# Performance work log

Measured on AMD Instinct MI355X. Metric: run time of the kernel, lower is better.

Reference implementation:

```python
import jax, jax.numpy as jnp
import numpy as np

B, T, E, H, D, NL = 2, 1024, 2048, 16, 128, 3
MAXL = T * (2 ** (NL - 1))  # k length doubles each layer: T, 2T, 4T


def _rms_norm(x, w, eps=1e-5):
    return x * jax.lax.rsqrt(jnp.mean(x * x, axis=-1, keepdims=True) + eps) * w


def _rope(x, cos, sin):
    # x: [B, S, H, D]; cos/sin: [>=S, D/2]; GPT-NeoX style (non-interleaved)
    S = x.shape[1]
    c = cos[:S][None, :, None, :]
    s = sin[:S][None, :, None, :]
    x1, x2 = jnp.split(x, 2, axis=-1)
    return jnp.concatenate([x1 * c - x2 * s, x1 * s + x2 * c], axis=-1)


def _causal_attn(q, k, v):
    # bottom-right-aligned causal (flash_attn_func causal=True with kv longer than q)
    Tq, L = q.shape[1], k.shape[1]
    scale = 1.0 / np.sqrt(q.shape[-1]).astype(np.float32)
    scores = jnp.einsum('bthd,bshd->bhts', q, k) * scale
    i = jnp.arange(Tq)[:, None]
    j = jnp.arange(L)[None, :]
    mask = j <= i + (L - Tq)
    scores = jnp.where(mask[None, None], scores, -jnp.inf)
    p = jax.nn.softmax(scores, axis=-1)
    return jnp.einsum('bhts,bshd->bthd', p, v)


def setup_inputs() -> dict:
    key = jax.random.key(0)
    ks = jax.random.split(key, 6)
    x = jax.random.normal(ks[0], (B, T, E), dtype=jnp.float32)
    inv_freq = 1.0 / (10000.0 ** (np.arange(0, D, 2, dtype=np.float32) / D))  # [D/2]
    ang = np.arange(MAXL, dtype=np.float32)[:, None] * inv_freq[None, :]      # [MAXL, D/2]
    cos = jnp.asarray(np.cos(ang), dtype=jnp.float32)
    sin = jnp.asarray(np.sin(ang), dtype=jnp.float32)
    wq = jax.random.normal(ks[1], (NL, E, E), dtype=jnp.float32) * 0.02
    wk = jax.random.normal(ks[2], (NL, E, E), dtype=jnp.float32) * 0.02
    wv = jax.random.normal(ks[3], (NL, E, E), dtype=jnp.float32) * 0.02
    ln_w = jnp.ones((NL, E), dtype=jnp.float32)
    lambdas = jnp.zeros((NL,), dtype=jnp.float32)
    w_out = jax.random.normal(ks[4], (E, E), dtype=jnp.float32) * 0.02
    final_ln_w = jnp.ones((E,), dtype=jnp.float32)
    alpha = jnp.ones((1,), dtype=jnp.float32)
    return {'x': x, 'cos': cos, 'sin': sin, 'wq': wq, 'wk': wk, 'wv': wv,
            'ln_w': ln_w, 'lambdas': lambdas, 'w_out': w_out,
            'final_ln_w': final_ln_w, 'alpha': alpha}


def reference(x, cos, sin, wq, wk, wv, ln_w, lambdas, w_out, final_ln_w, alpha):
    bsz, tgt_len, embed_dim = x.shape
    # lambda weights: sigmoid then LayerNorm over the NL scalars (no affine)
    lam = jax.nn.sigmoid(lambdas)
    lam = (lam - jnp.mean(lam)) * jax.lax.rsqrt(jnp.var(lam) + 1e-5)
    acc_k, acc_v = [], []
    total = jnp.zeros_like(x)
    for i in range(NL):  # small fixed layer count
        q = (x @ wq[i].T).reshape(bsz, tgt_len, H, D)
        k = (x @ wk[i].T).reshape(bsz, tgt_len, H, D)
        v = (x @ wv[i].T).reshape(bsz, tgt_len, H, D)
        if i > 0:
            k = jnp.concatenate([k] + acc_k, axis=1)
            v = jnp.concatenate([v] + acc_v, axis=1)
        q = _rope(q, cos, sin)
        k = _rope(k, cos, sin)  # note: cached K gets rotary re-applied, as in source
        attn = _causal_attn(q, k, v).reshape(bsz, tgt_len, embed_dim)
        attn = _rms_norm(attn, ln_w[i])
        total = total + attn * lam[i]
        acc_k.append(k)
        acc_v.append(v)
    out = _rms_norm(total + alpha * x, final_ln_w)
    return out @ w_out.T
```

## Files before the change

### kernel.cpp

```cpp
#include <hip/hip_runtime.h>
#include <hip/hip_bf16.h>

typedef unsigned short ushort_t;
typedef __attribute__((ext_vector_type(8))) short bf16x8;
typedef __attribute__((ext_vector_type(4))) short bf16x4;
typedef __attribute__((ext_vector_type(4))) float f32x4;
typedef __attribute__((ext_vector_type(4))) unsigned short u16x4;
typedef __attribute__((ext_vector_type(4))) unsigned int u32x4;

#define DEV __device__ __forceinline__

DEV ushort_t f2bf(float f) {
  __hip_bfloat16 h = __float2bfloat16(f);
  return __builtin_bit_cast(unsigned short, h);
}
DEV float bf2f(ushort_t b) {
  union { float f; unsigned int u; } a; a.u = ((unsigned int)b) << 16;
  return a.f;
}
DEV void gload_lds16(const void* g, void* l) {
  __builtin_amdgcn_global_load_lds((const __attribute__((address_space(1))) void*)g,
                                   (__attribute__((address_space(3))) void*)l, 16, 0, 0);
}
DEV unsigned ldsaddr(const void* l) {
  return (unsigned)(unsigned long long)(const __attribute__((address_space(3))) void*)l;
}
template <int OFF>
DEV bf16x4 tr16o(unsigned a) {
  bf16x4 d;
  asm volatile("ds_read_b64_tr_b16 %0, %1 offset:%c2" : "=v"(d) : "v"(a), "i"(OFF));
  return d;
}
template <int OFF>
DEV bf16x8 ldsb128o(unsigned a) {
  bf16x8 d;
  asm volatile("ds_read_b128 %0, %1 offset:%c2" : "=v"(d) : "v"(a), "i"(OFF));
  return d;
}

__global__ __launch_bounds__(256) void f2b_kernel(const float* __restrict__ in,
                                                  ushort_t* __restrict__ out, int n) {
  int base = (blockIdx.x * 256 + threadIdx.x) * 4;
  if (base >= n) return;
  f32x4 v = *(const f32x4*)(in + base);
  u16x4 o;
  o.x = f2bf(v.x); o.y = f2bf(v.y); o.z = f2bf(v.z); o.w = f2bf(v.w);
  *(u16x4*)(out + base) = o;
}

__global__ __launch_bounds__(256) void f2b3_kernel(const float* __restrict__ a, const float* __restrict__ b,
                                                   const float* __restrict__ c, ushort_t* __restrict__ out) {
  int id = blockIdx.x * 256 + threadIdx.x;
  int sel = id >> 20, k = (id & 1048575) * 4;
  const float* src = sel == 0 ? a : sel == 1 ? b : c;
  f32x4 v = *(const f32x4*)(src + k);
  u16x4 o;
  o.x = f2bf(v.x); o.y = f2bf(v.y); o.z = f2bf(v.z); o.w = f2bf(v.w);
  *(u16x4*)(out + (size_t)sel * 4194304 + k) = o;
}

__global__ void lam_kernel(const float* __restrict__ lambdas, float* __restrict__ lam) {
  if (threadIdx.x == 0 && blockIdx.x == 0) {
    float l0 = 1.f / (1.f + __expf(-lambdas[0]));
    float l1 = 1.f / (1.f + __expf(-lambdas[1]));
    float l2 = 1.f / (1.f + __expf(-lambdas[2]));
    float mean = (l0 + l1 + l2) * (1.f / 3.f);
    float d0 = l0 - mean, d1 = l1 - mean, d2 = l2 - mean;
    float var = (d0 * d0 + d1 * d1 + d2 * d2) * (1.f / 3.f);
    float rs = rsqrtf(var + 1e-5f);
    lam[0] = d0 * rs; lam[1] = d1 * rs; lam[2] = d2 * rs;
  }
}

DEV void gemm_core(const ushort_t* __restrict__ A, const ushort_t* __restrict__ Bm,
                   ushort_t* lsA, ushort_t* lsB, int bm, int bn, int kbeg, int kend,
                   f32x4 (&acc)[4][4]) {
  const int K = 2048;
  int tid = threadIdx.x;
  int w = tid >> 6, lane = tid & 63;
  int g = lane >> 4, r = lane & 15;
  int wm = w >> 1, wn = w & 1;
#pragma unroll
  for (int i = 0; i < 4; ++i)
#pragma unroll
    for (int j = 0; j < 4; ++j) acc[i][j] = 0.f;

  for (int kk = kbeg; kk < kend; kk += 32) {
    __syncthreads();
#pragma unroll
    for (int j2 = 0; j2 < 2; ++j2) {
      int eb = w * 1024 + j2 * 512;
      int ebl = eb + lane * 8;
      int rr = ebl >> 5, cc = ebl & 31;
      gload_lds16(A + (size_t)(bm * 128 + rr) * K + kk + cc, lsA + eb);
      gload_lds16(Bm + (size_t)(bn * 128 + rr) * K + kk + cc, lsB + eb);
    }
    __syncthreads();
    bf16x8 af[4], bfr[4];
#pragma unroll
    for (int i = 0; i < 4; ++i)
      af[i] = *(const bf16x8*)(lsA + (wm * 64 + i * 16 + r) * 32 + g * 8);
#pragma unroll
    for (int j = 0; j < 4; ++j)
      bfr[j] = *(const bf16x8*)(lsB + (wn * 64 + j * 16 + r) * 32 + g * 8);
#pragma unroll
    for (int i = 0; i < 4; ++i)
#pragma unroll
      for (int j = 0; j < 4; ++j)
        acc[i][j] = __builtin_amdgcn_mfma_f32_16x16x32_bf16(af[i], bfr[j], acc[i][j], 0, 0, 0);
  }
}

#define MM(i, j)                                                                              \
  acc[i][j] = __builtin_amdgcn_mfma_f32_16x16x32_bf16(af[(i) & 3][0], bfr[j][0], acc[i][j], 0, 0, 0); \
  acc[i][j] = __builtin_amdgcn_mfma_f32_16x16x32_bf16(af[(i) & 3][1], bfr[j][1], acc[i][j], 0, 0, 0);

__global__ __launch_bounds__(512, 2) void gemm_qkv256(
    const ushort_t* __restrict__ A,
    const ushort_t* __restrict__ Bq, const ushort_t* __restrict__ Bk, const ushort_t* __restrict__ Bv,
    ushort_t* __restrict__ Cq, ushort_t* __restrict__ Ck, ushort_t* __restrict__ Cv, int Lkv) {
  __shared__ __align__(16) ushort_t lsA[32768];
  __shared__ __align__(16) ushort_t lsB[32768];
  const int NT = 32;

  int bid = (int)blockIdx.x;
  int swz = (bid & 7) * 24 + (bid >> 3);
  int bm = swz / 24;
  int rest = swz % 24;
  int sel = rest >> 3, bnc = rest & 7;
  const ushort_t* Bmat = (sel == 0) ? Bq : (sel == 1) ? Bk : Bv;
  ushort_t* C = (sel == 0) ? Cq : (sel == 1) ? Ck : Cv;
  int Lsel = (sel == 0) ? 1024 : Lkv;

  int tid = threadIdx.x;
  int wv = tid >> 6, lane = tid & 63;
  int wm = wv >> 2, wn = wv & 3;
  int g = lane >> 4, r = lane & 15;

  int row0 = tid >> 3, c0 = tid & 7;
  int colsw = (c0 ^ (row0 & 7)) * 8;
  const ushort_t* pA0 = A + (size_t)(bm * 256 + row0) * 2048 + colsw;
  const ushort_t* pB0 = Bmat + (size_t)(bnc * 256 + row0) * 2048 + colsw;
  ushort_t* dA = lsA + tid * 8;
  ushort_t* dB = lsB + tid * 8;

  auto SA = [&](int T, int hh) {
    const ushort_t* s = pA0 + (size_t)(hh * 128) * 2048 + (size_t)T * 64;
    ushort_t* d = dA + (T & 1) * 16384 + hh * 8192;
    gload_lds16(s, d);
    gload_lds16(s + (size_t)64 * 2048, d + 4096);
  };
  auto SB = [&](int T, int hh) {
    const ushort_t* s = pB0 + (size_t)(hh * 128) * 2048 + (size_t)T * 64;
    ushort_t* d = dB + (T & 1) * 16384 + hh * 8192;
    gload_lds16(s, d);
    gload_lds16(s + (size_t)64 * 2048, d + 4096);
  };

  unsigned xm = (unsigned)(r & 7);
  unsigned aAb = ldsaddr(lsA) + (unsigned)((wm * 128 + r) * 128);
  unsigned aA0b = aAb + ((((unsigned)g) ^ xm) << 4);
  unsigned aA1b = aAb + ((((unsigned)(4 + g)) ^ xm) << 4);
  unsigned aBb = ldsaddr(lsB) + (unsigned)((wn * 64 + r) * 128);
  unsigned aB0b = aBb + ((((unsigned)g) ^ xm) << 4);
  unsigned aB1b = aBb + ((((unsigned)(4 + g)) ^ xm) << 4);

  f32x4 acc[8][4];
#pragma unroll
  for (int i = 0; i < 8; ++i)
#pragma unroll
    for (int j = 0; j < 4; ++j) acc[i][j] = 0.f;
  bf16x8 af[4][2], bfr[4][2];

  SA(0, 0); SB(0, 0); SB(0, 1); SA(0, 1);
  SA(1, 0); SB(1, 0); SB(1, 1);
  asm volatile("s_waitcnt vmcnt(6)" ::: "memory");
  __builtin_amdgcn_s_barrier();
  __builtin_amdgcn_sched_barrier(0);

  for (int t = 0; t < NT; ++t) {
    unsigned cb = (unsigned)((t & 1) << 15);
    unsigned A0 = aA0b + cb, A1 = aA1b + cb, B0 = aB0b + cb, B1 = aB1b + cb;
    bool full = (t < NT - 2);
    af[0][0] = ldsb128o<0>(A0);     af[0][1] = ldsb128o<0>(A1);
    af[1][0] = ldsb128o<2048>(A0);  af[1][1] = ldsb128o<2048>(A1);
    af[2][0] = ldsb128o<4096>(A0);  af[2][1] = ldsb128o<4096>(A1);
    af[3][0] = ldsb128o<6144>(A0);  af[3][1] = ldsb128o<6144>(A1);
    bfr[0][0] = ldsb128o<0>(B0);    bfr[0][1] = ldsb128o<0>(B1);
    bfr[1][0] = ldsb128o<2048>(B0); bfr[1][1] = ldsb128o<2048>(B1);
    if (t + 1 < NT) SA(t + 1, 1);
    __builtin_amdgcn_s_barrier();
    asm volatile("s_waitcnt lgkmcnt(0)" ::: "memory");
    __builtin_amdgcn_sched_barrier(0);
    __builtin_amdgcn_s_setprio(1);
    MM(0, 0) MM(1, 0) MM(2, 0) MM(3, 0) MM(0, 1) MM(1, 1) MM(2, 1) MM(3, 1)
    __builtin_amdgcn_s_setprio(0);
    __builtin_amdgcn_sched_barrier(0);
    __builtin_amdgcn_s_barrier();
    bfr[2][0] = ldsb128o<4096>(B0); bfr[2][1] = ldsb128o<4096>(B1);
    bfr[3][0] = ldsb128o<6144>(B0); bfr[3][1] = ldsb128o<6144>(B1);
    if (full) SA(t + 2, 0);
    __builtin_amdgcn_s_barrier();
    asm volatile("s_waitcnt lgkmcnt(0)" ::: "memory");
    __builtin_amdgcn_sched_barrier(0);
    __builtin_amdgcn_s_setprio(1);
    MM(0, 2) MM(1, 2) MM(2, 2) MM(3, 2) MM(0, 3) MM(1, 3) MM(2, 3) MM(3, 3)
    __builtin_amdgcn_s_setprio(0);
    if (full) { asm volatile("s_waitcnt vmcnt(4)" ::: "memory"); }
    else      { asm volatile("s_waitcnt vmcnt(0)" ::: "memory"); }
    __builtin_amdgcn_sched_barrier(0);
    __builtin_amdgcn_s_barrier();
    af[0][0] = ldsb128o<8192>(A0);  af[0][1] = ldsb128o<8192>(A1);
    af[1][0] = ldsb128o<10240>(A0); af[1][1] = ldsb128o<10240>(A1);
    af[2][0] = ldsb128o<12288>(A0); af[2][1] = ldsb128o<12288>(A1);
    af[3][0] = ldsb128o<14336>(A0); af[3][1] = ldsb128o<14336>(A1);
    if (full) SB(t + 2, 0);
    __builtin_amdgcn_s_barrier();
    asm volatile("s_waitcnt lgkmcnt(0)" ::: "memory");
    __builtin_amdgcn_sched_barrier(0);
    __builtin_amdgcn_s_setprio(1);
    MM(4, 2) MM(5, 2) MM(6, 2) MM(7, 2) MM(4, 3) MM(5, 3) MM(6, 3) MM(7, 3)
    __builtin_amdgcn_s_setprio(0);
    __builtin_amdgcn_sched_barrier(0);
    __builtin_amdgcn_s_barrier();
    if (full) SB(t + 2, 1);
    __builtin_amdgcn_s_barrier();
    __builtin_amdgcn_s_setprio(1);
    MM(4, 0) MM(5, 0) MM(6, 0) MM(7, 0) MM(4, 1) MM(5, 1) MM(6, 1) MM(7, 1)
    __builtin_amdgcn_s_setprio(0);
    if (full) { asm volatile("s_waitcnt vmcnt(8)" ::: "memory"); }
    else      { asm volatile("s_waitcnt vmcnt(0)" ::: "memory"); }
    __builtin_amdgcn_sched_barrier(0);
    __builtin_amdgcn_s_barrier();
  }

  int prow = bm * 256 + wm * 128 + g * 4;
  int pcol = bnc * 256 + wn * 64 + r;
#pragma unroll
  for (int i = 0; i < 8; ++i)
#pragma unroll
    for (int j = 0; j < 4; ++j) {
      int col = pcol + j * 16;
#pragma unroll
      for (int tt = 0; tt < 4; ++tt) {
        int row = prow + i * 16 + tt;
        int b2 = row >> 10, t2 = row & 1023;
        C[(size_t)(b2 * Lsel + t2) * 2048 + col] = f2bf(acc[i][j][tt]);
      }
    }
}
#undef MM

__global__ __launch_bounds__(256) void gemm_bt_part(
    const ushort_t* __restrict__ A, const ushort_t* __restrict__ Bm, float* __restrict__ P) {
  __shared__ __align__(16) ushort_t lsA[4096];
  __shared__ __align__(16) ushort_t lsB[4096];
  int bn = blockIdx.x, bm = blockIdx.y, s = blockIdx.z;
  f32x4 acc[4][4];
  gemm_core(A, Bm, lsA, lsB, bm, bn, s * 1024, (s + 1) * 1024, acc);
  float* C = P + (size_t)s * 4194304;
  int lane = threadIdx.x & 63, w = threadIdx.x >> 6;
  int g = lane >> 4, r = lane & 15, wm = w >> 1, wn = w & 1;
#pragma unroll
  for (int i = 0; i < 4; ++i)
#pragma unroll
    for (int j = 0; j < 4; ++j) {
      int row0 = bm * 128 + wm * 64 + i * 16 + g * 4;
      int col = bn * 128 + wn * 64 + j * 16 + r;
#pragma unroll
      for (int t = 0; t < 4; ++t)
        C[(size_t)(row0 + t) * 2048 + col] = acc[i][j][t];
    }
}

__global__ __launch_bounds__(256) void add2_kernel(const float* __restrict__ a, const float* __restrict__ b,
                                                   float* __restrict__ out) {
  int i = (blockIdx.x * 256 + threadIdx.x) * 4;
  f32x4 va = *(const f32x4*)(a + i);
  f32x4 vb = *(const f32x4*)(b + i);
  f32x4 r;
#pragma unroll
  for (int k = 0; k < 4; ++k) r[k] = va[k] + vb[k];
  *(f32x4*)(out + i) = r;
}

DEV void rope_body(const ushort_t* src, ushort_t* dst, const float* cosT, const float* sinT,
                   int Ls, int s0, int Ld, int dpos0, int cnt, int bp) {
  int b = bp / cnt, pidx = bp % cnt;
  int pos = dpos0 + pidx;
  int pi = threadIdx.x * 4;
  int h = pi >> 6, d = pi & 63;
  const ushort_t* s_ = src + ((size_t)(b * Ls + s0 + pidx) * 16 + h) * 128 + d;
  ushort_t* d_ = dst + ((size_t)(b * Ld + pos) * 16 + h) * 128 + d;
  f32x4 c4 = *(const f32x4*)(cosT + (size_t)pos * 64 + d);
  f32x4 s4 = *(const f32x4*)(sinT + (size_t)pos * 64 + d);
  u16x4 x1 = *(const u16x4*)(s_);
  u16x4 x2 = *(const u16x4*)(s_ + 64);
  u16x4 o1, o2;
#pragma unroll
  for (int k = 0; k < 4; ++k) {
    float a = bf2f(x1[k]), bb = bf2f(x2[k]);
    o1[k] = f2bf(a * c4[k] - bb * s4[k]);
    o2[k] = f2bf(a * s4[k] + bb * c4[k]);
  }
  *(u16x4*)d_ = o1;
  *(u16x4*)(d_ + 64) = o2;
}
DEV void copy_body(const ushort_t* src, ushort_t* dst, int Ls, int s0, int Ld, int dpos0,
                   int cnt, int bp) {
  int b = bp / cnt, pidx = bp % cnt;
  const u32x4* s = (const u32x4*)(src + (size_t)(b * Ls + s0 + pidx) * 2048);
  u32x4* d = (u32x4*)(dst + (size_t)(b * Ld + dpos0 + pidx) * 2048);
  d[threadIdx.x] = s[threadIdx.x];
}

__global__ __launch_bounds__(256) void rope_k(ushort_t* Kc, const float* __restrict__ cosT,
                                              const float* __restrict__ sinT, int L) {
  rope_body(Kc, Kc, cosT, sinT, L, 0, L, 0, 1024, blockIdx.x);
}

__global__ __launch_bounds__(256) void layer1_cache(const ushort_t* __restrict__ K0, ushort_t* __restrict__ K1,
                                                    const ushort_t* __restrict__ V0, ushort_t* __restrict__ V1,
                                                    const float* __restrict__ cosT, const float* __restrict__ sinT) {
  int bp = blockIdx.x;
  if (bp < 2048) rope_body(K0, K1, cosT, sinT, 1024, 0, 2048, 1024, 1024, bp);
  else copy_body(V0, V1, 1024, 0, 2048, 1024, 1024, bp - 2048);
}

__global__ __launch_bounds__(256) void layer2_cache(const ushort_t* __restrict__ K1, ushort_t* __restrict__ K2,
                                                    const ushort_t* __restrict__ V1, ushort_t* __restrict__ V2,
                                                    const float* __restrict__ cosT, const float* __restrict__ sinT) {
  int bp = blockIdx.x;
  if (bp < 2048) copy_body(K1, K2, 2048, 1024, 4096, 1024, 1024, bp);
  else if (bp < 6144) rope_body(K1, K2, cosT, sinT, 2048, 0, 4096, 2048, 2048, bp - 2048);
  else if (bp < 8192) copy_body(V1, V2, 2048, 1024, 4096, 1024, 1024, bp - 6144);
  else copy_body(V1, V2, 2048, 0, 4096, 2048, 2048, bp - 8192);
}

__global__ __launch_bounds__(256, 4) void attn_kernel(
    const ushort_t* __restrict__ Qraw, const ushort_t* __restrict__ Kc, const ushort_t* __restrict__ Vc,
    const float* __restrict__ cosT, const float* __restrict__ sinT,
    ushort_t* __restrict__ Opart, float2* __restrict__ Ml, int Lk) {
  __shared__ __align__(16) ushort_t lsK[8192];
  __shared__ __align__(16) ushort_t lsV[8192];
  const float SC2 = 0.1275174366f;

  int bid = (int)blockIdx.x;
  int swz = (bid & 7) * 128 + (bid >> 3);
  int s = swz & 1;
  int rest = swz >> 1;

  int w = threadIdx.x >> 6, lane = threadIdx.x & 63;
  int bq = rest & 15, h = (rest >> 4) & 15, b = rest >> 8;
  int qt = bq * 4 + w;
  int g = lane >> 4, r = lane & 15;
  int off = Lk - 1024;

  const ushort_t* qbase = Qraw + ((size_t)(b * 1024 + qt * 16 + r) * 16 + h) * 128;
  int pos = qt * 16 + r;
  const float* cb = cosT + (size_t)pos * 64;
  const float* sb = sinT + (size_t)pos * 64;
  bf16x8 qf[4];
#pragma unroll
  for (int c = 0; c < 2; ++c) {
    int d0 = c * 32 + g * 8;
    f32x4 c0 = *(const f32x4*)(cb + d0);
    f32x4 c1 = *(const f32x4*)(cb + d0 + 4);
    f32x4 s0 = *(const f32x4*)(sb + d0);
    f32x4 s1 = *(const f32x4*)(sb + d0 + 4);
    bf16x8 x1 = *(const bf16x8*)(qbase + d0);
    bf16x8 x2 = *(const bf16x8*)(qbase + d0 + 64);
    bf16x8 lo, hi;
#pragma unroll
    for (int k = 0; k < 8; ++k) {
      float cv = (k < 4 ? c0[k] : c1[k - 4]) * SC2;
      float sv = (k < 4 ? s0[k] : s1[k - 4]) * SC2;
      float a = bf2f((ushort_t)x1[k]);
      float bb = bf2f((ushort_t)x2[k]);
      lo[k] = (short)f2bf(a * cv - bb * sv);
      hi[k] = (short)f2bf(a * sv + bb * cv);
    }
    qf[c] = lo; qf[c + 2] = hi;
  }

  int t = threadIdx.x;
  int krow0 = t >> 4,        kc0 = (t & 15) ^ (krow0 & 7);
  int krow1 = (t + 256) >> 4, kc1 = (t & 15) ^ (krow1 & 7);
  const size_t adv = 32 * 2048;
  const size_t adv2 = 2 * adv;
  const ushort_t* srcK0 = Kc + ((size_t)(b * Lk + krow0) * 16 + h) * 128 + kc0 * 8 + s * adv;
  const ushort_t* srcK1 = Kc + ((size_t)(b * Lk + krow1) * 16 + h) * 128 + kc1 * 8 + s * adv;
  int L0 = t, L1 = t + 256;
  int vrow0 = ((L0 >> 3) & 7) * 4 + ((L0 >> 1) & 3), vd0 = (L0 >> 6) * 16 + (L0 & 1) * 8;
  int vrow1 = ((L1 >> 3) & 7) * 4 + ((L1 >> 1) & 3), vd1 = (L1 >> 6) * 16 + (L1 & 1) * 8;
  const ushort_t* srcV0 = Vc + ((size_t)(b * Lk + vrow0) * 16 + h) * 128 + vd0 + s * adv;
  const ushort_t* srcV1 = Vc + ((size_t)(b * Lk + vrow1) * 16 + h) * 128 + vd1 + s * adv;

  auto STAGE = [&](int buf) {
    ushort_t* k0 = lsK + buf * 4096 + w * 512;
    ushort_t* v0 = lsV + buf * 4096 + w * 512;
    gload_lds16(srcK0, k0);
    gload_lds16(srcK1, k0 + 2048);
    gload_lds16(srcV0, v0);
    gload_lds16(srcV1, v0 + 2048);
    srcK0 += adv2; srcK1 += adv2; srcV0 += adv2; srcV1 += adv2;
  };

  unsigned kx[4];
  unsigned kbase0 = ldsaddr(lsK) + (unsigned)(r * 256);
#pragma unroll
  for (int c = 0; c < 4; ++c)
    kx[c] = kbase0 + (unsigned)((((c * 32 + g * 8) ^ ((r & 7) * 8))) * 2);
  unsigned vbase0 = ldsaddr(lsV);

  float m_run = -1e30f, l_run = 0.f;
  f32x4 o[8];
#pragma unroll
  for (int c = 0; c < 8; ++c) o[c] = 0.f;

  int qp = qt * 16 + r + off;
  int qmin = qt * 16 + off;
  int nkt_w = ((qt * 16 + 15 + off) >> 5) + 1;
  int nkt_blk = (((bq * 4 + 3) * 16 + 15 + off) >> 5) + 1;
  int ntile = (nkt_blk - s + 1) >> 1;

#define LDK(c, ks) ldsb128o<(ks) * 4096>(kx[c] + kb)
#define LDV(hh, i) tr16o<(hh) * 4096 + (i) * 512>(vb)

  if (ntile > 0) {
    STAGE(0);
    for (int it = 0; it < ntile; ++it) {
      int kt = s + it * 2;
      int cur = it & 1;
      if (it + 1 < ntile) {
        STAGE(cur ^ 1);
        asm volatile("s_waitcnt vmcnt(4)" ::: "memory");
      } else {
        asm volatile("s_waitcnt vmcnt(0)" ::: "memory");
      }
      __builtin_amdgcn_s_barrier();
      __builtin_amdgcn_sched_barrier(0);
      if (kt < nkt_w) {
        unsigned kb = (unsigned)(cur << 13);
        unsigned vb = vbase0 + kb;
        f32x4 st[2];
        {
          bf16x8 k0 = LDK(0, 0), k1 = LDK(1, 0), k2 = LDK(2, 0), k3 = LDK(3, 0);
          asm volatile("s_waitcnt lgkmcnt(0)" ::: "memory");
          __builtin_amdgcn_sched_barrier(0);
          __builtin_amdgcn_s_setprio(1);
          f32x4 acc = 0.f;
          acc = __builtin_amdgcn_mfma_f32_16x16x32_bf16(k0, qf[0], acc, 0, 0, 0);
          acc = __builtin_amdgcn_mfma_f32_16x16x32_bf16(k1, qf[1], acc, 0, 0, 0);
          acc = __builtin_amdgcn_mfma_f32_16x16x32_bf16(k2, qf[2], acc, 0, 0, 0);
          acc = __builtin_amdgcn_mfma_f32_16x16x32_bf16(k3, qf[3], acc, 0, 0, 0);
          __builtin_amdgcn_s_setprio(0);
          st[0] = acc;
        }
        {
          bf16x8 k0 = LDK(0, 1), k1 = LDK(1, 1), k2 = LDK(2, 1), k3 = LDK(3, 1);
          asm volatile("s_waitcnt lgkmcnt(0)" ::: "memory");
          __builtin_amdgcn_sched_barrier(0);
          __builtin_amdgcn_s_setprio(1);
          f32x4 acc = 0.f;
          acc = __builtin_amdgcn_mfma_f32_16x16x32_bf16(k0, qf[0], acc, 0, 0, 0);
          acc = __builtin_amdgcn_mfma_f32_16x16x32_bf16(k1, qf[1], acc, 0, 0, 0);
          acc = __builtin_amdgcn_mfma_f32_16x16x32_bf16(k2, qf[2], acc, 0, 0, 0);
          acc = __builtin_amdgcn_mfma_f32_16x16x32_bf16(k3, qf[3], acc, 0, 0, 0);
          __builtin_amdgcn_s_setprio(0);
          st[1] = acc;
        }
        float pmax = -1e30f;
        int kp0 = kt * 32;
        if (kp0 + 31 > qmin) {
#pragma unroll
          for (int ks = 0; ks < 2; ++ks)
#pragma unroll
            for (int j = 0; j < 4; ++j) {
              int key = kp0 + ks * 16 + g * 4 + j;
              float sv = st[ks][j];
              if (key > qp) sv = -1e30f;
              st[ks][j] = sv;
              pmax = fmaxf(pmax, sv);
            }
        } else {
#pragma unroll
          for (int ks = 0; ks < 2; ++ks)
#pragma unroll
            for (int j = 0; j < 4; ++j) pmax = fmaxf(pmax, st[ks][j]);
        }
        pmax = fmaxf(pmax, __shfl_xor(pmax, 16, 64));
        pmax = fmaxf(pmax, __shfl_xor(pmax, 32, 64));
        if (!__all(pmax <= m_run + 11.5f)) {
          float mnew = fmaxf(m_run, pmax);
          float corr = exp2f(m_run - mnew);
          l_run *= corr;
#pragma unroll
          for (int c = 0; c < 8; ++c)
#pragma unroll
            for (int tt = 0; tt < 4; ++tt) o[c][tt] *= corr;
          m_run = mnew;
        }
        float psum = 0.f;
        bf16x4 pf[2];
#pragma unroll
        for (int ks = 0; ks < 2; ++ks)
#pragma unroll
          for (int j = 0; j < 4; ++j) {
            float pe = exp2f(st[ks][j] - m_run);
            psum += pe;
            pf[ks][j] = (short)f2bf(pe);
          }
        psum += __shfl_xor(psum, 16, 64);
        psum += __shfl_xor(psum, 32, 64);
        l_run += psum;
        {
          bf16x4 v0 = LDV(0, 0), v1 = LDV(0, 1), v2 = LDV(0, 2), v3 = LDV(0, 3);
          bf16x4 v4 = LDV(0, 4), v5 = LDV(0, 5), v6 = LDV(0, 6), v7 = LDV(0, 7);
          asm volatile("s_waitcnt lgkmcnt(0)" ::: "memory");
          __builtin_amdgcn_sched_barrier(0);
          __builtin_amdgcn_s_setprio(1);
          o[0] = __builtin_amdgcn_mfma_f32_16x16x16bf16_1k(v0, pf[0], o[0], 0, 0, 0);
          o[0] = __builtin_amdgcn_mfma_f32_16x16x16bf16_1k(v1, pf[1], o[0], 0, 0, 0);
          o[1] = __builtin_amdgcn_mfma_f32_16x16x16bf16_1k(v2, pf[0], o[1], 0, 0, 0);
          o[1] = __builtin_amdgcn_mfma_f32_16x16x16bf16_1k(v3, pf[1], o[1], 0, 0, 0);
          o[2] = __builtin_amdgcn_mfma_f32_16x16x16bf16_1k(v4, pf[0], o[2], 0, 0, 0);
          o[2] = __builtin_amdgcn_mfma_f32_16x16x16bf16_1k(v5, pf[1], o[2], 0, 0, 0);
          o[3] = __builtin_amdgcn_mfma_f32_16x16x16bf16_1k(v6, pf[0], o[3], 0, 0, 0);
          o[3] = __builtin_amdgcn_mfma_f32_16x16x16bf16_1k(v7, pf[1], o[3], 0, 0, 0);
          __builtin_amdgcn_s_setprio(0);
        }
        {
          bf16x4 v0 = LDV(1, 0), v1 = LDV(1, 1), v2 = LDV(1, 2), v3 = LDV(1, 3);
          bf16x4 v4 = LDV(1, 4), v5 = LDV(1, 5), v6 = LDV(1, 6), v7 = LDV(1, 7);
          asm volatile("s_waitcnt lgkmcnt(0)" ::: "memory");
          __builtin_amdgcn_sched_barrier(0);
          __builtin_amdgcn_s_setprio(1);
          o[4] = __builtin_amdgcn_mfma_f32_16x16x16bf16_1k(v0, pf[0], o[4], 0, 0, 0);
          o[4] = __builtin_amdgcn_mfma_f32_16x16x16bf16_1k(v1, pf[1], o[4], 0, 0, 0);
          o[5] = __builtin_amdgcn_mfma_f32_16x16x16bf16_1k(v2, pf[0], o[5], 0, 0, 0);
          o[5] = __builtin_amdgcn_mfma_f32_16x16x16bf16_1k(v3, pf[1], o[5], 0, 0, 0);
          o[6] = __builtin_amdgcn_mfma_f32_16x16x16bf16_1k(v4, pf[0], o[6], 0, 0, 0);
          o[6] = __builtin_amdgcn_mfma_f32_16x16x16bf16_1k(v5, pf[1], o[6], 0, 0, 0);
          o[7] = __builtin_amdgcn_mfma_f32_16x16x16bf16_1k(v6, pf[0], o[7], 0, 0, 0);
          o[7] = __builtin_amdgcn_mfma_f32_16x16x16bf16_1k(v7, pf[1], o[7], 0, 0, 0);
          __builtin_amdgcn_s_setprio(0);
        }
      }
      __builtin_amdgcn_sched_barrier(0);
      __builtin_amdgcn_s_barrier();
    }
  }
#undef LDK
#undef LDV
  ushort_t* ob = Opart + (size_t)s * 4194304 + ((size_t)(b * 1024 + qt * 16 + r) * 16 + h) * 128;
#pragma unroll
  for (int dblk = 0; dblk < 8; ++dblk) {
    u16x4 ov;
#pragma unroll
    for (int tt = 0; tt < 4; ++tt) ov[tt] = f2bf(o[dblk][tt]);
    *(u16x4*)(ob + dblk * 16 + g * 4) = ov;
  }
  if (g == 0) {
    float2 ml; ml.x = m_run; ml.y = l_run;
    Ml[((size_t)(s * 2 + b) * 1024 + qt * 16 + r) * 16 + h] = ml;
  }
}

template <int FIRST>
__global__ __launch_bounds__(256) void rms_combine(const ushort_t* __restrict__ Opart, const float2* __restrict__ Ml,
                                                   const float* __restrict__ lnw, const float* __restrict__ lam,
                                                   int li, float* __restrict__ total) {
  int row = blockIdx.x;
  int t8 = threadIdx.x * 8;
  int h = t8 >> 7;
  float2 ml0 = Ml[(size_t)row * 16 + h];
  float2 ml1 = Ml[(size_t)(row + 2048) * 16 + h];
  float M = fmaxf(ml0.x, ml1.x);
  float w0 = exp2f(ml0.x - M), w1 = exp2f(ml1.x - M);
  float rinv = 1.f / (w0 * ml0.y + w1 * ml1.y);
  w0 *= rinv; w1 *= rinv;
  const ushort_t* a0 = Opart + (size_t)row * 2048 + t8;
  const ushort_t* a1 = a0 + 4194304;
  u16x4 p00 = *(const u16x4*)(a0);
  u16x4 p01 = *(const u16x4*)(a0 + 4);
  u16x4 p10 = *(const u16x4*)(a1);
  u16x4 p11 = *(const u16x4*)(a1 + 4);
  f32x4 v0, v1;
#pragma unroll
  for (int k = 0; k < 4; ++k) {
    v0[k] = w0 * bf2f(p00[k]) + w1 * bf2f(p10[k]);
    v1[k] = w0 * bf2f(p01[k]) + w1 * bf2f(p11[k]);
  }
  float ss = v0.x * v0.x + v0.y * v0.y + v0.z * v0.z + v0.w * v0.w +
             v1.x * v1.x + v1.y * v1.y + v1.z * v1.z + v1.w * v1.w;
#pragma unroll
  for (int m = 1; m < 64; m <<= 1) ss += __shfl_xor(ss, m, 64);
  __shared__ float red[4];
  int w = threadIdx.x >> 6, lane = threadIdx.x & 63;
  if (lane == 0) red[w] = ss;
  __syncthreads();
  ss = red[0] + red[1] + red[2] + red[3];
  float sca = rsqrtf(ss * (1.f / 2048.f) + 1e-5f) * lam[li];
  f32x4 w0v = *(const f32x4*)(lnw + t8);
  f32x4 w1v = *(const f32x4*)(lnw + t8 + 4);
  float* o = total + (size_t)row * 2048 + t8;
  f32x4 r0, r1;
#pragma unroll
  for (int k = 0; k < 4; ++k) { r0[k] = v0[k] * sca * w0v[k]; r1[k] = v1[k] * sca * w1v[k]; }
  if (!FIRST) {
    f32x4 q0 = *(const f32x4*)(o);
    f32x4 q1 = *(const f32x4*)(o + 4);
#pragma unroll
    for (int k = 0; k < 4; ++k) { r0[k] += q0[k]; r1[k] += q1[k]; }
  }
  *(f32x4*)(o) = r0;
  *(f32x4*)(o + 4) = r1;
}

__global__ __launch_bounds__(256) void final_norm(const float* __restrict__ total, const float* __restrict__ x,
                                                  const float* __restrict__ alphap, const float* __restrict__ flw,
                                                  ushort_t* __restrict__ ybf) {
  int row = blockIdx.x;
  float al = alphap[0];
  int t8 = threadIdx.x * 8;
  const float* tp = total + (size_t)row * 2048 + t8;
  const float* xp = x + (size_t)row * 2048 + t8;
  f32x4 t0 = *(const f32x4*)(tp);
  f32x4 t1 = *(const f32x4*)(tp + 4);
  f32x4 x0 = *(const f32x4*)(xp);
  f32x4 x1 = *(const f32x4*)(xp + 4);
  float y[8];
#pragma unroll
  for (int k = 0; k < 4; ++k) { y[k] = t0[k] + al * x0[k]; y[4 + k] = t1[k] + al * x1[k]; }
  float ss = 0.f;
#pragma unroll
  for (int k = 0; k < 8; ++k) ss += y[k] * y[k];
#pragma unroll
  for (int m = 1; m < 64; m <<= 1) ss += __shfl_xor(ss, m, 64);
  __shared__ float red[4];
  int w = threadIdx.x >> 6, lane = threadIdx.x & 63;
  if (lane == 0) red[w] = ss;
  __syncthreads();
  ss = red[0] + red[1] + red[2] + red[3];
  float s = rsqrtf(ss * (1.f / 2048.f) + 1e-5f);
  f32x4 w0 = *(const f32x4*)(flw + t8);
  f32x4 w1 = *(const f32x4*)(flw + t8 + 4);
  u16x4 o0, o1;
#pragma unroll
  for (int k = 0; k < 4; ++k) {
    o0[k] = f2bf(y[k] * s * w0[k]);
    o1[k] = f2bf(y[4 + k] * s * w1[k]);
  }
  *(u16x4*)(ybf + (size_t)row * 2048 + t8) = o0;
  *(u16x4*)(ybf + (size_t)row * 2048 + t8 + 4) = o1;
}

extern "C" void kernel_launch(void* const* d_in, const int* in_sizes, int n_in,
                              void* d_out, int out_size, void* d_ws, size_t ws_size,
                              hipStream_t stream) {
  const float* x = (const float*)d_in[0];
  const float* cosT = (const float*)d_in[1];
  const float* sinT = (const float*)d_in[2];
  const float* wq = (const float*)d_in[3];
  const float* wk = (const float*)d_in[4];
  const float* wv = (const float*)d_in[5];
  const float* lnw = (const float*)d_in[6];
  const float* lambdas = (const float*)d_in[7];
  const float* w_out = (const float*)d_in[8];
  const float* flw = (const float*)d_in[9];
  const float* alpha = (const float*)d_in[10];

  const size_t ME = 4194304ull;
  char* p = (char*)d_ws;
  size_t off = 0;
  auto alc = [&](size_t bytes) -> void* {
    void* r = p + off;
    off += (bytes + 255) & ~(size_t)255;
    return r;
  };
  ushort_t* xb = (ushort_t*)alc(ME * 2);
  void* uni = alc(2 * ME * 4);
  ushort_t* wl = (ushort_t*)uni;
  ushort_t* Opart = (ushort_t*)uni;
  float* Ppart = (float*)uni;
  ushort_t* q = (ushort_t*)alc(ME * 2);
  ushort_t* K0 = (ushort_t*)alc(ME * 2);
  ushort_t* K1 = (ushort_t*)alc(2 * ME * 2);
  ushort_t* K2 = (ushort_t*)alc(4 * ME * 2);
  ushort_t* V0 = (ushort_t*)alc(ME * 2);
  ushort_t* V1 = (ushort_t*)alc(2 * ME * 2);
  ushort_t* V2 = (ushort_t*)alc(4 * ME * 2);
  float* total = (float*)alc(ME * 4);
  float2* Ml = (float2*)alc(65536 * 8);
  float* lam = (float*)alc(256);
  ushort_t* ybf = q;
  ushort_t* wob = K0;

  f2b_kernel<<<4096, 256, 0, stream>>>(x, xb, 4194304);
  lam_kernel<<<1, 64, 0, stream>>>(lambdas, lam);

  ushort_t* Kc[3] = {K0, K1, K2};
  ushort_t* Vc[3] = {V0, V1, V2};

  for (int li = 0; li < 3; ++li) {
    int L = 1024 << li;
    size_t woff = (size_t)li * ME;
    f2b3_kernel<<<12288, 256, 0, stream>>>(wq + woff, wk + woff, wv + woff, wl);
    gemm_qkv256<<<192, 512, 0, stream>>>(xb, wl, wl + ME, wl + 2 * ME,
                                         q, Kc[li], Vc[li], L);
    rope_k<<<2048, 256, 0, stream>>>(Kc[li], cosT, sinT, L);
    if (li == 1)
      layer1_cache<<<4096, 256, 0, stream>>>(K0, K1, V0, V1, cosT, sinT);
    else if (li == 2)
      layer2_cache<<<12288, 256, 0, stream>>>(K1, K2, V1, V2, cosT, sinT);
    attn_kernel<<<1024, 256, 0, stream>>>(q, Kc[li], Vc[li], cosT, sinT, Opart, Ml, L);
    if (li == 0)
      rms_combine<1><<<2048, 256, 0, stream>>>(Opart, Ml, lnw, lam, 0, total);
    else
      rms_combine<0><<<2048, 256, 0, stream>>>(Opart, Ml, lnw + (size_t)li * 2048, lam, li, total);
  }

  f2b_kernel<<<4096, 256, 0, stream>>>(w_out, wob, 4194304);
  final_norm<<<2048, 256, 0, stream>>>(total, x, alpha, flw, ybf);
  gemm_bt_part<<<dim3(16, 16, 2), 256, 0, stream>>>(ybf, wob, Ppart);
  add2_kernel<<<4096, 256, 0, stream>>>(Ppart, Ppart + ME, (float*)d_out);
}
```

Measured before the change: 543.1 us.

## Split attention KV tiles three ways and combine three partials

The attention kernel now interleaves key tiles across three split groups instead of two, launching 1536 blocks with an occupancy hint of 5 blocks per CU. The rms_combine kernel merges three partial outputs and their softmax max/sum pairs, and the Ml buffer is enlarged to hold them. The cross-lane max shuffle in the online-softmax rescale check is also deferred so it runs only when some lane's local max exceeds the threshold. The aim is more parallelism and better load balance for the causal workload. The cost is extra partial-output traffic in the combine step, possible register pressure from the tighter launch bound, and a partial last wave of blocks.

```diff
diff --git a/kernel.cpp b/kernel.cpp
--- a/kernel.cpp
+++ b/kernel.cpp
@@ -337,7 +337,7 @@
   else copy_body(V1, V2, 2048, 0, 4096, 2048, 2048, bp - 8192);
 }
 
-__global__ __launch_bounds__(256, 4) void attn_kernel(
+__global__ __launch_bounds__(256, 5) void attn_kernel(
     const ushort_t* __restrict__ Qraw, const ushort_t* __restrict__ Kc, const ushort_t* __restrict__ Vc,
     const float* __restrict__ cosT, const float* __restrict__ sinT,
     ushort_t* __restrict__ Opart, float2* __restrict__ Ml, int Lk) {
@@ -346,9 +346,9 @@
   const float SC2 = 0.1275174366f;
 
   int bid = (int)blockIdx.x;
-  int swz = (bid & 7) * 128 + (bid >> 3);
-  int s = swz & 1;
-  int rest = swz >> 1;
+  int swz = (bid & 7) * 192 + (bid >> 3);
+  int s = swz % 3;
+  int rest = swz / 3;
 
   int w = threadIdx.x >> 6, lane = threadIdx.x & 63;
   int bq = rest & 15, h = (rest >> 4) & 15, b = rest >> 8;
@@ -387,7 +387,7 @@
   int krow0 = t >> 4,        kc0 = (t & 15) ^ (krow0 & 7);
   int krow1 = (t + 256) >> 4, kc1 = (t & 15) ^ (krow1 & 7);
   const size_t adv = 32 * 2048;
-  const size_t adv2 = 2 * adv;
+  const size_t adv3 = 3 * adv;
   const ushort_t* srcK0 = Kc + ((size_t)(b * Lk + krow0) * 16 + h) * 128 + kc0 * 8 + s * adv;
   const ushort_t* srcK1 = Kc + ((size_t)(b * Lk + krow1) * 16 + h) * 128 + kc1 * 8 + s * adv;
   int L0 = t, L1 = t + 256;
@@ -403,7 +403,7 @@
     gload_lds16(srcK1, k0 + 2048);
     gload_lds16(srcV0, v0);
     gload_lds16(srcV1, v0 + 2048);
-    srcK0 += adv2; srcK1 += adv2; srcV0 += adv2; srcV1 += adv2;
+    srcK0 += adv3; srcK1 += adv3; srcV0 += adv3; srcV1 += adv3;
   };
 
   unsigned kx[4];
@@ -422,7 +422,7 @@
   int qmin = qt * 16 + off;
   int nkt_w = ((qt * 16 + 15 + off) >> 5) + 1;
   int nkt_blk = (((bq * 4 + 3) * 16 + 15 + off) >> 5) + 1;
-  int ntile = (nkt_blk - s + 1) >> 1;
+  int ntile = (nkt_blk - s + 2) / 3;
 
 #define LDK(c, ks) ldsb128o<(ks) * 4096>(kx[c] + kb)
 #define LDV(hh, i) tr16o<(hh) * 4096 + (i) * 512>(vb)
@@ -430,7 +430,7 @@
   if (ntile > 0) {
     STAGE(0);
     for (int it = 0; it < ntile; ++it) {
-      int kt = s + it * 2;
+      int kt = s + it * 3;
       int cur = it & 1;
       if (it + 1 < ntile) {
         STAGE(cur ^ 1);
@@ -470,7 +470,7 @@
           __builtin_amdgcn_s_setprio(0);
           st[1] = acc;
         }
-        float pmax = -1e30f;
+        float pmaxl = -1e30f;
         int kp0 = kt * 32;
         if (kp0 + 31 > qmin) {
 #pragma unroll
@@ -481,25 +481,27 @@
               float sv = st[ks][j];
               if (key > qp) sv = -1e30f;
               st[ks][j] = sv;
-              pmax = fmaxf(pmax, sv);
+              pmaxl = fmaxf(pmaxl, sv);
             }
         } else {
 #pragma unroll
           for (int ks = 0; ks < 2; ++ks)
 #pragma unroll
-            for (int j = 0; j < 4; ++j) pmax = fmaxf(pmax, st[ks][j]);
+            for (int j = 0; j < 4; ++j) pmaxl = fmaxf(pmaxl, st[ks][j]);
         }
-        pmax = fmaxf(pmax, __shfl_xor(pmax, 16, 64));
-        pmax = fmaxf(pmax, __shfl_xor(pmax, 32, 64));
-        if (!__all(pmax <= m_run + 11.5f)) {
-          float mnew = fmaxf(m_run, pmax);
-          float corr = exp2f(m_run - mnew);
-          l_run *= corr;
-#pragma unroll
-          for (int c = 0; c < 8; ++c)
-#pragma unroll
-            for (int tt = 0; tt < 4; ++tt) o[c][tt] *= corr;
-          m_run = mnew;
+        if (!__all(pmaxl <= m_run + 11.5f)) {
+          float pmax = fmaxf(pmaxl, __shfl_xor(pmaxl, 16, 64));
+          pmax = fmaxf(pmax, __shfl_xor(pmax, 32, 64));
+          if (pmax > m_run + 11.5f) {
+            float mnew = fmaxf(m_run, pmax);
+            float corr = exp2f(m_run - mnew);
+            l_run *= corr;
+#pragma unroll
+            for (int c = 0; c < 8; ++c)
+#pragma unroll
+              for (int tt = 0; tt < 4; ++tt) o[c][tt] *= corr;
+            m_run = mnew;
+          }
         }
         float psum = 0.f;
         bf16x4 pf[2];
@@ -576,21 +578,25 @@
   int h = t8 >> 7;
   float2 ml0 = Ml[(size_t)row * 16 + h];
   float2 ml1 = Ml[(size_t)(row + 2048) * 16 + h];
-  float M = fmaxf(ml0.x, ml1.x);
-  float w0 = exp2f(ml0.x - M), w1 = exp2f(ml1.x - M);
-  float rinv = 1.f / (w0 * ml0.y + w1 * ml1.y);
-  w0 *= rinv; w1 *= rinv;
+  float2 ml2 = Ml[(size_t)(row + 4096) * 16 + h];
+  float M = fmaxf(fmaxf(ml0.x, ml1.x), ml2.x);
+  float w0 = exp2f(ml0.x - M), w1 = exp2f(ml1.x - M), w2 = exp2f(ml2.x - M);
+  float rinv = 1.f / (w0 * ml0.y + w1 * ml1.y + w2 * ml2.y);
+  w0 *= rinv; w1 *= rinv; w2 *= rinv;
   const ushort_t* a0 = Opart + (size_t)row * 2048 + t8;
   const ushort_t* a1 = a0 + 4194304;
+  const ushort_t* a2 = a0 + 2 * 4194304;
   u16x4 p00 = *(const u16x4*)(a0);
   u16x4 p01 = *(const u16x4*)(a0 + 4);
   u16x4 p10 = *(const u16x4*)(a1);
   u16x4 p11 = *(const u16x4*)(a1 + 4);
+  u16x4 p20 = *(const u16x4*)(a2);
+  u16x4 p21 = *(const u16x4*)(a2 + 4);
   f32x4 v0, v1;
 #pragma unroll
   for (int k = 0; k < 4; ++k) {
-    v0[k] = w0 * bf2f(p00[k]) + w1 * bf2f(p10[k]);
-    v1[k] = w0 * bf2f(p01[k]) + w1 * bf2f(p11[k]);
+    v0[k] = w0 * bf2f(p00[k]) + w1 * bf2f(p10[k]) + w2 * bf2f(p20[k]);
+    v1[k] = w0 * bf2f(p01[k]) + w1 * bf2f(p11[k]) + w2 * bf2f(p21[k]);
   }
   float ss = v0.x * v0.x + v0.y * v0.y + v0.z * v0.z + v0.w * v0.w +
              v1.x * v1.x + v1.y * v1.y + v1.z * v1.z + v1.w * v1.w;
@@ -692,7 +698,7 @@
   ushort_t* V1 = (ushort_t*)alc(2 * ME * 2);
   ushort_t* V2 = (ushort_t*)alc(4 * ME * 2);
   float* total = (float*)alc(ME * 4);
-  float2* Ml = (float2*)alc(65536 * 8);
+  float2* Ml = (float2*)alc(98304 * 8);
   float* lam = (float*)alc(256);
   ushort_t* ybf = q;
   ushort_t* wob = K0;
@@ -714,7 +720,7 @@
       layer1_cache<<<4096, 256, 0, stream>>>(K0, K1, V0, V1, cosT, sinT);
     else if (li == 2)
       layer2_cache<<<12288, 256, 0, stream>>>(K1, K2, V1, V2, cosT, sinT);
-    attn_kernel<<<1024, 256, 0, stream>>>(q, Kc[li], Vc[li], cosT, sinT, Opart, Ml, L);
+    attn_kernel<<<1536, 256, 0, stream>>>(q, Kc[li], Vc[li], cosT, sinT, Opart, Ml, L);
     if (li == 0)
       rms_combine<1><<<2048, 256, 0, stream>>>(Opart, Ml, lnw, lam, 0, total);
     else
```

Measured after the change: 848.4 us. 1.56x slower.

## Write V cache copies from GEMM epilogue and skip redundant cache copy kernels

Applied to the files above, without the earlier changes.

The QKV GEMM epilogue now also writes the V projection straight into its slots in the later layers' V caches. The layer-1 K rope step writes to both K1 and K2, so the separate copy passes over V and K in the cache kernels are removed. This cuts global memory read and write traffic and block counts in the cache-building kernels. In exchange the GEMM epilogue does extra scattered stores. Separately, in attention the cross-lane max reduction is now skipped when every lane's local max is within the rescale threshold.

```diff
diff --git a/kernel.cpp b/kernel.cpp
--- a/kernel.cpp
+++ b/kernel.cpp
@@ -118,7 +118,10 @@
 __global__ __launch_bounds__(512, 2) void gemm_qkv256(
     const ushort_t* __restrict__ A,
     const ushort_t* __restrict__ Bq, const ushort_t* __restrict__ Bk, const ushort_t* __restrict__ Bv,
-    ushort_t* __restrict__ Cq, ushort_t* __restrict__ Ck, ushort_t* __restrict__ Cv, int Lkv) {
+    ushort_t* __restrict__ Cq, ushort_t* __restrict__ Ck, ushort_t* __restrict__ Cv, int Lkv,
+    ushort_t* __restrict__ ve0, size_t vs0,
+    ushort_t* __restrict__ ve1, size_t vs1,
+    ushort_t* __restrict__ ve2, size_t vs2) {
   __shared__ __align__(16) ushort_t lsA[32768];
   __shared__ __align__(16) ushort_t lsB[32768];
   const int NT = 32;
@@ -245,7 +248,14 @@
       for (int tt = 0; tt < 4; ++tt) {
         int row = prow + i * 16 + tt;
         int b2 = row >> 10, t2 = row & 1023;
-        C[(size_t)(b2 * Lsel + t2) * 2048 + col] = f2bf(acc[i][j][tt]);
+        ushort_t val = f2bf(acc[i][j][tt]);
+        C[(size_t)(b2 * Lsel + t2) * 2048 + col] = val;
+        if (sel == 2) {
+          size_t rc = (size_t)t2 * 2048 + col;
+          if (ve0) ve0[(size_t)b2 * vs0 + rc] = val;
+          if (ve1) ve1[(size_t)b2 * vs1 + rc] = val;
+          if (ve2) ve2[(size_t)b2 * vs2 + rc] = val;
+        }
       }
     }
 }
@@ -306,13 +316,6 @@
   *(u16x4*)d_ = o1;
   *(u16x4*)(d_ + 64) = o2;
 }
-DEV void copy_body(const ushort_t* src, ushort_t* dst, int Ls, int s0, int Ld, int dpos0,
-                   int cnt, int bp) {
-  int b = bp / cnt, pidx = bp % cnt;
-  const u32x4* s = (const u32x4*)(src + (size_t)(b * Ls + s0 + pidx) * 2048);
-  u32x4* d = (u32x4*)(dst + (size_t)(b * Ld + dpos0 + pidx) * 2048);
-  d[threadIdx.x] = s[threadIdx.x];
-}
 
 __global__ __launch_bounds__(256) void rope_k(ushort_t* Kc, const float* __restrict__ cosT,
                                               const float* __restrict__ sinT, int L) {
@@ -320,21 +323,37 @@
 }
 
 __global__ __launch_bounds__(256) void layer1_cache(const ushort_t* __restrict__ K0, ushort_t* __restrict__ K1,
-                                                    const ushort_t* __restrict__ V0, ushort_t* __restrict__ V1,
+                                                    ushort_t* __restrict__ K2,
                                                     const float* __restrict__ cosT, const float* __restrict__ sinT) {
   int bp = blockIdx.x;
-  if (bp < 2048) rope_body(K0, K1, cosT, sinT, 1024, 0, 2048, 1024, 1024, bp);
-  else copy_body(V0, V1, 1024, 0, 2048, 1024, 1024, bp - 2048);
+  int b = bp >> 10, pidx = bp & 1023;
+  int pos = 1024 + pidx;
+  int pi = threadIdx.x * 4;
+  int h = pi >> 6, d = pi & 63;
+  size_t io = ((size_t)h) * 128 + d;
+  const ushort_t* s_ = K0 + ((size_t)(b * 1024 + pidx) * 16) * 128 + io;
+  ushort_t* d1 = K1 + ((size_t)(b * 2048 + pos) * 16) * 128 + io;
+  ushort_t* d2 = K2 + ((size_t)(b * 4096 + pos) * 16) * 128 + io;
+  f32x4 c4 = *(const f32x4*)(cosT + (size_t)pos * 64 + d);
+  f32x4 s4 = *(const f32x4*)(sinT + (size_t)pos * 64 + d);
+  u16x4 x1 = *(const u16x4*)(s_);
+  u16x4 x2 = *(const u16x4*)(s_ + 64);
+  u16x4 o1, o2;
+#pragma unroll
+  for (int k = 0; k < 4; ++k) {
+    float a = bf2f(x1[k]), bb = bf2f(x2[k]);
+    o1[k] = f2bf(a * c4[k] - bb * s4[k]);
+    o2[k] = f2bf(a * s4[k] + bb * c4[k]);
+  }
+  *(u16x4*)d1 = o1;
+  *(u16x4*)(d1 + 64) = o2;
+  *(u16x4*)d2 = o1;
+  *(u16x4*)(d2 + 64) = o2;
 }
 
 __global__ __launch_bounds__(256) void layer2_cache(const ushort_t* __restrict__ K1, ushort_t* __restrict__ K2,
-                                                    const ushort_t* __restrict__ V1, ushort_t* __restrict__ V2,
                                                     const float* __restrict__ cosT, const float* __restrict__ sinT) {
-  int bp = blockIdx.x;
-  if (bp < 2048) copy_body(K1, K2, 2048, 1024, 4096, 1024, 1024, bp);
-  else if (bp < 6144) rope_body(K1, K2, cosT, sinT, 2048, 0, 4096, 2048, 2048, bp - 2048);
-  else if (bp < 8192) copy_body(V1, V2, 2048, 1024, 4096, 1024, 1024, bp - 6144);
-  else copy_body(V1, V2, 2048, 0, 4096, 2048, 2048, bp - 8192);
+  rope_body(K1, K2, cosT, sinT, 2048, 0, 4096, 2048, 2048, blockIdx.x);
 }
 
 __global__ __launch_bounds__(256, 4) void attn_kernel(
@@ -470,7 +489,7 @@
           __builtin_amdgcn_s_setprio(0);
           st[1] = acc;
         }
-        float pmax = -1e30f;
+        float pmaxl = -1e30f;
         int kp0 = kt * 32;
         if (kp0 + 31 > qmin) {
 #pragma unroll
@@ -481,25 +500,27 @@
               float sv = st[ks][j];
               if (key > qp) sv = -1e30f;
               st[ks][j] = sv;
-              pmax = fmaxf(pmax, sv);
+              pmaxl = fmaxf(pmaxl, sv);
             }
         } else {
 #pragma unroll
           for (int ks = 0; ks < 2; ++ks)
 #pragma unroll
-            for (int j = 0; j < 4; ++j) pmax = fmaxf(pmax, st[ks][j]);
+            for (int j = 0; j < 4; ++j) pmaxl = fmaxf(pmaxl, st[ks][j]);
         }
-        pmax = fmaxf(pmax, __shfl_xor(pmax, 16, 64));
-        pmax = fmaxf(pmax, __shfl_xor(pmax, 32, 64));
-        if (!__all(pmax <= m_run + 11.5f)) {
-          float mnew = fmaxf(m_run, pmax);
-          float corr = exp2f(m_run - mnew);
-          l_run *= corr;
-#pragma unroll
-          for (int c = 0; c < 8; ++c)
-#pragma unroll
-            for (int tt = 0; tt < 4; ++tt) o[c][tt] *= corr;
-          m_run = mnew;
+        if (!__all(pmaxl <= m_run + 11.5f)) {
+          float pmax = fmaxf(pmaxl, __shfl_xor(pmaxl, 16, 64));
+          pmax = fmaxf(pmax, __shfl_xor(pmax, 32, 64));
+          if (pmax > m_run + 11.5f) {
+            float mnew = fmaxf(m_run, pmax);
+            float corr = exp2f(m_run - mnew);
+            l_run *= corr;
+#pragma unroll
+            for (int c = 0; c < 8; ++c)
+#pragma unroll
+              for (int tt = 0; tt < 4; ++tt) o[c][tt] *= corr;
+            m_run = mnew;
+          }
         }
         float psum = 0.f;
         bf16x4 pf[2];
@@ -702,18 +723,30 @@
 
   ushort_t* Kc[3] = {K0, K1, K2};
   ushort_t* Vc[3] = {V0, V1, V2};
+  const size_t S2 = (size_t)2048 * 2048;
+  const size_t S4 = (size_t)4096 * 2048;
 
   for (int li = 0; li < 3; ++li) {
     int L = 1024 << li;
     size_t woff = (size_t)li * ME;
     f2b3_kernel<<<12288, 256, 0, stream>>>(wq + woff, wk + woff, wv + woff, wl);
+    ushort_t *ve0 = nullptr, *ve1 = nullptr, *ve2 = nullptr;
+    size_t vs0 = 0, vs1 = 0, vs2 = 0;
+    if (li == 0) {
+      ve0 = V1 + (size_t)1024 * 2048; vs0 = S2;
+      ve1 = V2 + (size_t)1024 * 2048; vs1 = S4;
+      ve2 = V2 + (size_t)3072 * 2048; vs2 = S4;
+    } else if (li == 1) {
+      ve0 = V2 + (size_t)2048 * 2048; vs0 = S4;
+    }
     gemm_qkv256<<<192, 512, 0, stream>>>(xb, wl, wl + ME, wl + 2 * ME,
-                                         q, Kc[li], Vc[li], L);
+                                         q, Kc[li], Vc[li], L,
+                                         ve0, vs0, ve1, vs1, ve2, vs2);
     rope_k<<<2048, 256, 0, stream>>>(Kc[li], cosT, sinT, L);
     if (li == 1)
-      layer1_cache<<<4096, 256, 0, stream>>>(K0, K1, V0, V1, cosT, sinT);
+      layer1_cache<<<2048, 256, 0, stream>>>(K0, K1, K2, cosT, sinT);
     else if (li == 2)
-      layer2_cache<<<12288, 256, 0, stream>>>(K1, K2, V1, V2, cosT, sinT);
+      layer2_cache<<<4096, 256, 0, stream>>>(K1, K2, cosT, sinT);
     attn_kernel<<<1024, 256, 0, stream>>>(q, Kc[li], Vc[li], cosT, sinT, Opart, Ml, L);
     if (li == 0)
       rms_combine<1><<<2048, 256, 0, stream>>>(Opart, Ml, lnw, lam, 0, total);
```

New measurement: 555.4 us. +2.2%, slower.
